# Kernel optimization log

Hardware: AMD Instinct MI355X
Metric: run time of the kernel (lower is better)

The kernel has to match this reference:

```python
import jax, jax.numpy as jnp
import numpy as np

NEG_SLOPE = 0.01
K = 27  # 3x3x3 kernel taps


def conv3d(x, w, b, pad):
    out = jax.lax.conv_general_dilated(
        x, w, window_strides=(1, 1, 1), padding=[(pad, pad)] * 3,
        dimension_numbers=('NCDHW', 'OIDHW', 'NCDHW'))
    return out + b[None, :, None, None, None]


def lrelu(v):
    return jnp.where(v >= 0, v, NEG_SLOPE * v)


def deform_conv3d_hw(x, offsets, w, b):
    # x: [B,C,T,H,W]; offsets: [B,2*K,T,H,W] with (dh, dw) per kernel tap;
    # depth offset is 0 ('HW' mode). Bilinear sampling in H,W, zero pad OOB.
    B, C, T, H, W = x.shape
    off = offsets.reshape(B, K, 2, T, H, W)
    dh, dw = off[:, :, 0], off[:, :, 1]  # [B,K,T,H,W]
    kidx = jnp.arange(K)
    kt = (kidx // 9)[None, :, None, None, None]
    kh = ((kidx // 3) % 3)[None, :, None, None, None]
    kw = (kidx % 3)[None, :, None, None, None]

    t_in = jnp.arange(T)[None, None, :, None, None] - 1 + kt           # int, [1,K,T,1,1]
    h_s = (jnp.arange(H)[None, None, None, :, None] - 1 + kh) + dh     # [B,K,T,H,W]
    w_s = (jnp.arange(W)[None, None, None, None, :] - 1 + kw) + dw

    t_ok = (t_in >= 0) & (t_in < T)
    t_c = jnp.clip(t_in, 0, T - 1)
    t_idx = jnp.broadcast_to(t_c, (B, K, T, H, W))
    t_ok = jnp.broadcast_to(t_ok, (B, K, T, H, W))

    h0 = jnp.floor(h_s); w0 = jnp.floor(w_s)
    fh = h_s - h0; fw = w_s - w0
    h0i = h0.astype(jnp.int32); w0i = w0.astype(jnp.int32)

    def gather_b(xb, ti, hi, wi):
        return xb[:, ti, hi, wi]  # [C,K,T,H,W]
    gather = jax.vmap(gather_b)

    cols = jnp.zeros((B, C, K, T, H, W), x.dtype)
    for ih, wgt_h in ((h0i, 1.0 - fh), (h0i + 1, fh)):
        h_ok = (ih >= 0) & (ih < H)
        ih_c = jnp.clip(ih, 0, H - 1)
        for iw, wgt_w in ((w0i, 1.0 - fw), (w0i + 1, fw)):
            w_ok = (iw >= 0) & (iw < W)
            iw_c = jnp.clip(iw, 0, W - 1)
            mask = (t_ok & h_ok & w_ok).astype(x.dtype)
            wgt = (wgt_h * wgt_w * mask)[:, None]  # [B,1,K,T,H,W]
            cols = cols + wgt * gather(x, t_idx, ih_c, iw_c)
    O = w.shape[0]
    out = jnp.einsum('bckthw,ock->bothw', cols, w.reshape(O, C, K))
    return out + b[None, :, None, None, None]


def setup_inputs() -> dict:
    key = jax.random.key(0)
    ks = jax.random.split(key, 9)
    B, Cin, Cout, T, H, W = 1, 64, 64, 8, 64, 64
    s1 = 1.0 / np.sqrt(Cin * 27)
    sr = 1.0 / np.sqrt(Cin)
    sd = 1.0 / np.sqrt(Cout * 27)
    return {
        'x': jax.random.normal(ks[0], (B, Cin, T, H, W), jnp.float32),
        'W1': jax.random.normal(ks[1], (Cout, Cin, 3, 3, 3), jnp.float32) * s1,
        'b1': jax.random.normal(ks[2], (Cout,), jnp.float32) * s1,
        'W_off': jax.random.normal(ks[3], (2 * K, Cout, 3, 3, 3), jnp.float32) * 0.01,
        'b_off': jax.random.normal(ks[4], (2 * K,), jnp.float32) * 0.01,
        'Wd': jax.random.normal(ks[5], (Cout, Cout, 3, 3, 3), jnp.float32) * sd,
        'bd': jax.random.normal(ks[6], (Cout,), jnp.float32) * sd,
        'Wr': jax.random.normal(ks[7], (Cout, Cin, 1, 1, 1), jnp.float32) * sr,
        'br': jax.random.normal(ks[8], (Cout,), jnp.float32) * sr,
    }


def reference(x, W1, b1, W_off, b_off, Wd, bd, Wr, br):
    y1 = lrelu(conv3d(x, W1, b1, pad=1))
    offsets = conv3d(y1, W_off, b_off, pad=1)          # DeformConvPack offset branch
    y2 = lrelu(deform_conv3d_hw(y1, offsets, Wd, bd))  # deformable conv, 'HW' offsets
    res = conv3d(x, Wr, br, pad=0)                     # 1x1x1 residual conv
    return y2 + res
```

## Files before the change

kernel.cpp:

```cpp
#include <hip/hip_runtime.h>
#include <hip/hip_bf16.h>

#define T_ 8
#define H_ 64
#define W_ 64
#define C_ 64
#define HW_ (H_ * W_)
#define THW_ (T_ * H_ * W_)
#define KTAPS 27
#define KDIM (C_ * KTAPS)
#define NOFF 54
#define OSTR2 58
#define AWC 35
#define AWCP 36

typedef __bf16 bf16x8 __attribute__((ext_vector_type(8)));
typedef float floatx4 __attribute__((ext_vector_type(4)));

#define LGKM_BARRIER()                                        \
    do {                                                      \
        asm volatile("s_waitcnt lgkmcnt(0)" ::: "memory");    \
        __builtin_amdgcn_s_barrier();                         \
    } while (0)

#define DECODE_SWZ_CONV(bid, t, h, wh)                        \
    const int hi3_ = (bid) & 7;                               \
    const int rest_ = (bid) >> 3;                             \
    const int wh = rest_ & 1;                                 \
    const int h = hi3_ * 8 + ((rest_ >> 1) & 7);              \
    const int t = rest_ >> 4;
#define DECODE_SWZ_ROW(bid, t, h)                             \
    const int h = ((bid) & 7) * 8 + (((bid) >> 3) & 7);       \
    const int t = (bid) >> 6;

__global__ __launch_bounds__(256) void prep_tocl_kernel(
    const float* __restrict__ x, __hip_bfloat16* __restrict__ xcl,
    const float* __restrict__ w1, const float* __restrict__ woff,
    const float* __restrict__ wd, const float* __restrict__ wr,
    __hip_bfloat16* __restrict__ w1s, __hip_bfloat16* __restrict__ woffs,
    __hip_bfloat16* __restrict__ wds, __hip_bfloat16* __restrict__ wrs) {
    __shared__ float tile[64][65];
    const int tid = threadIdx.x;

    {
        int i = blockIdx.x * 256 + tid;
        if (i < C_ * KDIM) {
            int j = i & 7, lane = (i >> 3) & 63, s = (i >> 9) & 1, g16 = (i >> 10) & 3, tap = i >> 12;
            int co = g16 * 16 + (lane & 15);
            int cin = s * 32 + (lane >> 4) * 8 + j;
            int src = (co * C_ + cin) * KTAPS + tap;
            w1s[i] = __float2bfloat16(w1[src]);
            woffs[i] = (co < NOFF) ? __float2bfloat16(woff[src]) : __float2bfloat16(0.f);
            wds[i] = __float2bfloat16(wd[src]);
        }
        if (i < C_ * C_) {
            int j = i & 7, lane = (i >> 3) & 63, s = (i >> 9) & 1, g16 = i >> 10;
            int co = g16 * 16 + (lane & 15);
            int cin = s * 32 + (lane >> 4) * 8 + j;
            wrs[i] = __float2bfloat16(wr[co * C_ + cin]);
        }
    }

    const int pos0 = blockIdx.x * 64;
    for (int i = tid; i < 4096; i += 256) {
        int ch = i >> 6, p = i & 63;
        tile[ch][p] = x[ch * THW_ + pos0 + p];
    }
    __syncthreads();
    for (int i = tid; i < 4096; i += 256) {
        int p = i >> 6, ch = i & 63;
        xcl[(pos0 + p) * C_ + ch] = __float2bfloat16(tile[ch][p]);
    }
}

__global__ __launch_bounds__(256) void conv_stream_kernel(
    const __hip_bfloat16* __restrict__ in_cl,
    const __hip_bfloat16* __restrict__ wTs,
    const float* __restrict__ bias,
    __hip_bfloat16* __restrict__ out_cl_b16) {
    __shared__ __hip_bfloat16 ts[32 * 72];
    __shared__ __hip_bfloat16 awin[3 * AWCP * C_];

    const int tid = threadIdx.x;
    const int wv = tid >> 6;
    const int lane = tid & 63;
    const int l15 = lane & 15;
    const int quad = lane >> 4;
    DECODE_SWZ_CONV(blockIdx.x, t, h, wh)
    const int w0 = wh * 32;
    const int pg = wv >> 1;
    const int chf = wv & 1;
    const int wpos = w0 + pg * 16 + l15;
    const int posbase = t * HW_ + h * W_;

    floatx4 acc0 = (floatx4){0.f, 0.f, 0.f, 0.f};
    floatx4 acc1 = (floatx4){0.f, 0.f, 0.f, 0.f};
    const bf16x8 z = {};
    const __hip_bfloat16* wb = wTs + chf * 2048 + lane * 8;

    auto rdwin = [&](int rr, int cc, int chunk) -> bf16x8 {
        const int u = (rr * AWCP + cc) * 8 + (chunk ^ (cc & 7));
        return *(const bf16x8*)((const char*)awin + u * 16);
    };

    const int ktlo = (t == 0) ? 1 : 0;
    const int kthi = (t == T_ - 1) ? 2 : 3;

#pragma unroll 1
    for (int kt = ktlo; kt < kthi; ++kt) {
        const int t_in = t - 1 + kt;

        LGKM_BARRIER();
        for (int i = tid; i < 3 * AWC * 8; i += 256) {
            const int rh = i / (AWC * 8);
            const int rem = i - rh * (AWC * 8);
            const int rw = rem >> 3;
            const int cc = rem & 7;
            const int hsrc = min(max(h - 1 + rh, 0), H_ - 1);
            const int wsrc = min(max(w0 - 1 + rw, 0), W_ - 1);
            const int u = (rh * AWCP + rw) * 8 + (cc ^ (rw & 7));
            *(bf16x8*)((char*)awin + u * 16) =
                *(const bf16x8*)&in_cl[(t_in * HW_ + hsrc * W_ + wsrc) * C_ + cc * 8];
        }
        LGKM_BARRIER();

#pragma unroll 1
        for (int kh = 0; kh < 3; ++kh) {
            const int h_in = h - 1 + kh;
            if ((unsigned)h_in >= H_) continue;
#pragma unroll
            for (int kw = 0; kw < 3; ++kw) {
                const int tap = kt * 9 + kh * 3 + kw;
                const int w_in = wpos - 1 + kw;
                const bool v = (unsigned)w_in < W_;
                const int rw = pg * 16 + l15 + kw;
                bf16x8 a0 = rdwin(kh, rw, quad);
                bf16x8 a1 = rdwin(kh, rw, quad + 4);
                a0 = v ? a0 : z;
                a1 = v ? a1 : z;
                const __hip_bfloat16* bp = wb + tap * 4096;
                const bf16x8 b00 = *(const bf16x8*)(bp);
                const bf16x8 b01 = *(const bf16x8*)(bp + 512);
                const bf16x8 b10 = *(const bf16x8*)(bp + 1024);
                const bf16x8 b11 = *(const bf16x8*)(bp + 1536);
                acc0 = __builtin_amdgcn_mfma_f32_16x16x32_bf16(a0, b00, acc0, 0, 0, 0);
                acc0 = __builtin_amdgcn_mfma_f32_16x16x32_bf16(a1, b01, acc0, 0, 0, 0);
                acc1 = __builtin_amdgcn_mfma_f32_16x16x32_bf16(a0, b10, acc1, 0, 0, 0);
                acc1 = __builtin_amdgcn_mfma_f32_16x16x32_bf16(a1, b11, acc1, 0, 0, 0);
            }
        }
    }

    const int n0 = chf * 32 + l15;
    const float bv0 = bias[n0], bv1 = bias[n0 + 16];
#pragma unroll
    for (int r = 0; r < 4; ++r) {
        const int p = pg * 16 + quad * 4 + r;
        float v0 = acc0[r] + bv0;
        v0 = (v0 >= 0.f) ? v0 : 0.01f * v0;
        float v1 = acc1[r] + bv1;
        v1 = (v1 >= 0.f) ? v1 : 0.01f * v1;
        ts[p * 72 + n0] = __float2bfloat16(v0);
        ts[p * 72 + n0 + 16] = __float2bfloat16(v1);
    }
    __syncthreads();
    {
        const int p = tid >> 3, ck = tid & 7;
        const uint4 v4 = *(const uint4*)&ts[p * 72 + ck * 8];
        *(uint4*)&out_cl_b16[(posbase + w0 + p) * C_ + ck * 8] = v4;
    }
}

struct G2 {
    bf16x8 a[4];
    bf16x8 b[4];
    float w00, w01, w10, w11;
};

__global__ __launch_bounds__(256) void deform_fused_kernel(
    const __hip_bfloat16* __restrict__ y1b,
    const __hip_bfloat16* __restrict__ woffs, const float* __restrict__ boff,
    const __hip_bfloat16* __restrict__ wds, const float* __restrict__ bd,
    const __hip_bfloat16* __restrict__ xclb, const __hip_bfloat16* __restrict__ wrs,
    const float* __restrict__ br, float* __restrict__ out) {
    __shared__ __hip_bfloat16 win[6 * 64 * 64];
    __shared__ float offs[4][16][OSTR2];

    const int tid = threadIdx.x;
    const int wv = tid >> 6;
    const int lane = tid & 63;
    const int l15 = lane & 15;
    const int quad = lane >> 4;
    DECODE_SWZ_ROW(blockIdx.x, t, h)
    const int posbase = t * HW_ + h * W_;
    const int pw = wv * 16 + l15;

    const int ktlo = (t == 0) ? 1 : 0;
    const int kthi = (t == T_ - 1) ? 2 : 3;

    auto rdwin = [&](int rr, int cc, int chunk) -> bf16x8 {
        const int u = (rr * 64 + cc) * 8 + (chunk ^ (cc & 7));
        return *(const bf16x8*)((const char*)win + u * 16);
    };

    {
        floatx4 oacc[4];
#pragma unroll
        for (int g = 0; g < 4; ++g) oacc[g] = (floatx4){0.f, 0.f, 0.f, 0.f};
        const bf16x8 z = {};

#pragma unroll 1
        for (int kt = ktlo; kt < kthi; ++kt) {
            const int tin = t - 1 + kt;

            LGKM_BARRIER();
            for (int i = tid; i < 3 * 64 * 8; i += 256) {
                const int rh = i >> 9;
                const int rem = i & 511;
                const int rw = rem >> 3;
                const int cc = rem & 7;
                const int hsrc = min(max(h - 1 + rh, 0), H_ - 1);
                const int u = (rh * 64 + rw) * 8 + (cc ^ (rw & 7));
                *(bf16x8*)((char*)win + u * 16) =
                    *(const bf16x8*)&y1b[(tin * HW_ + hsrc * W_ + rw) * C_ + cc * 8];
            }
            LGKM_BARRIER();

#pragma unroll 1
            for (int kh = 0; kh < 3; ++kh) {
                const int h_in = h - 1 + kh;
                if ((unsigned)h_in >= H_) continue;
#pragma unroll
                for (int kw = 0; kw < 3; ++kw) {
                    const int tap = kt * 9 + kh * 3 + kw;
                    const int w_in = pw - 1 + kw;
                    const bool v = (unsigned)w_in < W_;
                    const int wc = v ? w_in : 0;
                    bf16x8 a0 = rdwin(kh, wc, quad);
                    bf16x8 a1 = rdwin(kh, wc, quad + 4);
                    a0 = v ? a0 : z;
                    a1 = v ? a1 : z;
                    const __hip_bfloat16* op = woffs + tap * 4096 + lane * 8;
#pragma unroll
                    for (int g = 0; g < 4; ++g) {
                        const bf16x8 b0 = *(const bf16x8*)(op + g * 1024);
                        const bf16x8 b1 = *(const bf16x8*)(op + g * 1024 + 512);
                        oacc[g] = __builtin_amdgcn_mfma_f32_16x16x32_bf16(a0, b0, oacc[g], 0, 0, 0);
                        oacc[g] = __builtin_amdgcn_mfma_f32_16x16x32_bf16(a1, b1, oacc[g], 0, 0, 0);
                    }
                }
            }
        }
#pragma unroll
        for (int g = 0; g < 4; ++g) {
            const int idx = g * 16 + l15;
            if (idx < NOFF) {
                const float bo = boff[idx];
#pragma unroll
                for (int r = 0; r < 4; ++r)
                    offs[wv][quad * 4 + r][idx] = oacc[g][r] + bo;
            }
        }
    }

    floatx4 acc[4], racc[4];
#pragma unroll
    for (int g = 0; g < 4; ++g) {
        acc[g] = (floatx4){0.f, 0.f, 0.f, 0.f};
        racc[g] = (floatx4){0.f, 0.f, 0.f, 0.f};
    }

    {
        const __hip_bfloat16* ap = xclb + (posbase + pw) * C_ + quad * 8;
        const bf16x8 ra0 = *(const bf16x8*)(ap);
        const bf16x8 ra1 = *(const bf16x8*)(ap + 32);
        const __hip_bfloat16* q = wrs + lane * 8;
#pragma unroll
        for (int g = 0; g < 4; ++g) {
            const bf16x8 r0 = *(const bf16x8*)(q + g * 1024);
            const bf16x8 r1 = *(const bf16x8*)(q + g * 1024 + 512);
            racc[g] = __builtin_amdgcn_mfma_f32_16x16x32_bf16(ra0, r0, racc[g], 0, 0, 0);
            racc[g] = __builtin_amdgcn_mfma_f32_16x16x32_bf16(ra1, r1, racc[g], 0, 0, 0);
        }
    }

    auto load_off = [&](int k, float& dh, float& dw) {
        dh = offs[wv][l15][2 * k];
        dw = offs[wv][l15][2 * k + 1];
    };
    auto gatherW = [&](int k, float dh, float dw, G2& g) {
        const int kh = (k / 3) % 3, kw = k % 3;
        const float hs = (float)(h - 1 + kh) + dh;
        const float wsv = (float)(pw - 1 + kw) + dw;
        const float h0f = floorf(hs), w0f = floorf(wsv);
        const float fh = hs - h0f, fw = wsv - w0f;
        const int h0i = (int)h0f, w0i = (int)w0f;
        const int h1i = h0i + 1, w1i = w0i + 1;
        const float m_h0 = ((unsigned)h0i < H_) ? 1.f : 0.f;
        const float m_h1 = ((unsigned)h1i < H_) ? 1.f : 0.f;
        const float m_w0 = ((unsigned)w0i < W_) ? 1.f : 0.f;
        const float m_w1 = ((unsigned)w1i < W_) ? 1.f : 0.f;
        g.w00 = (1.f - fh) * (1.f - fw) * m_h0 * m_w0;
        g.w01 = (1.f - fh) * fw * m_h0 * m_w1;
        g.w10 = fh * (1.f - fw) * m_h1 * m_w0;
        g.w11 = fh * fw * m_h1 * m_w1;
        const int w0c = min(max(w0i, 0), W_ - 1);
        const int w1c = min(max(w1i, 0), W_ - 1);
        const int rh = h0i - (h - 2);
        if ((unsigned)rh <= 4u) {
            g.a[0] = rdwin(rh, w0c, quad);      g.b[0] = rdwin(rh, w0c, quad + 4);
            g.a[1] = rdwin(rh, w1c, quad);      g.b[1] = rdwin(rh, w1c, quad + 4);
            g.a[2] = rdwin(rh + 1, w0c, quad);  g.b[2] = rdwin(rh + 1, w0c, quad + 4);
            g.a[3] = rdwin(rh + 1, w1c, quad);  g.b[3] = rdwin(rh + 1, w1c, quad + 4);
        } else {
            const int h0c = min(max(h0i, 0), H_ - 1);
            const int h1c = min(max(h1i, 0), H_ - 1);
            const int tb = (t - 1 + k / 9) * HW_;
            const __hip_bfloat16* p00 = y1b + (tb + h0c * W_ + w0c) * C_ + quad * 8;
            const __hip_bfloat16* p01 = y1b + (tb + h0c * W_ + w1c) * C_ + quad * 8;
            const __hip_bfloat16* p10 = y1b + (tb + h1c * W_ + w0c) * C_ + quad * 8;
            const __hip_bfloat16* p11 = y1b + (tb + h1c * W_ + w1c) * C_ + quad * 8;
            g.a[0] = *(const bf16x8*)(p00);  g.b[0] = *(const bf16x8*)(p00 + 32);
            g.a[1] = *(const bf16x8*)(p01);  g.b[1] = *(const bf16x8*)(p01 + 32);
            g.a[2] = *(const bf16x8*)(p10);  g.b[2] = *(const bf16x8*)(p10 + 32);
            g.a[3] = *(const bf16x8*)(p11);  g.b[3] = *(const bf16x8*)(p11 + 32);
        }
    };
    auto blend2 = [&](const G2& g, bf16x8& lo, bf16x8& hi) {
        union U { bf16x8 v; __hip_bfloat16 e[8]; };
        U c0, c1, c2, c3, r;
        c0.v = g.a[0]; c1.v = g.a[1]; c2.v = g.a[2]; c3.v = g.a[3];
#pragma unroll
        for (int j = 0; j < 8; ++j) {
            float f = g.w00 * __bfloat162float(c0.e[j]) + g.w01 * __bfloat162float(c1.e[j]) +
                      g.w10 * __bfloat162float(c2.e[j]) + g.w11 * __bfloat162float(c3.e[j]);
            r.e[j] = __float2bfloat16(f);
        }
        lo = r.v;
        c0.v = g.b[0]; c1.v = g.b[1]; c2.v = g.b[2]; c3.v = g.b[3];
#pragma unroll
        for (int j = 0; j < 8; ++j) {
            float f = g.w00 * __bfloat162float(c0.e[j]) + g.w01 * __bfloat162float(c1.e[j]) +
                      g.w10 * __bfloat162float(c2.e[j]) + g.w11 * __bfloat162float(c3.e[j]);
            r.e[j] = __float2bfloat16(f);
        }
        hi = r.v;
    };
    auto tapMFMA = [&](int k, const bf16x8& lo, const bf16x8& hi) {
        const __hip_bfloat16* q = wds + k * 4096 + lane * 8;
#pragma unroll
        for (int g = 0; g < 4; ++g) {
            const bf16x8 b0 = *(const bf16x8*)(q + g * 1024);
            const bf16x8 b1 = *(const bf16x8*)(q + g * 1024 + 512);
            acc[g] = __builtin_amdgcn_mfma_f32_16x16x32_bf16(lo, b0, acc[g], 0, 0, 0);
            acc[g] = __builtin_amdgcn_mfma_f32_16x16x32_bf16(hi, b1, acc[g], 0, 0, 0);
        }
    };

    G2 gA, gB;
#pragma unroll 1
    for (int kt = ktlo; kt < kthi; ++kt) {
        const int tin = t - 1 + kt;
        const int kg = kt * 9;

        LGKM_BARRIER();
        for (int i = tid; i < 6 * 64 * 8; i += 256) {
            const int rh = i >> 9;
            const int rem = i & 511;
            const int rw = rem >> 3;
            const int cc = rem & 7;
            const int hsrc = min(max(h - 2 + rh, 0), H_ - 1);
            const int u = (rh * 64 + rw) * 8 + (cc ^ (rw & 7));
            *(bf16x8*)((char*)win + u * 16) =
                *(const bf16x8*)&y1b[(tin * HW_ + hsrc * W_ + rw) * C_ + cc * 8];
        }
        LGKM_BARRIER();

        {
            float dh, dw;
            load_off(kg, dh, dw);
            gatherW(kg, dh, dw, gA);
        }
        int k = kg;
        for (; k + 1 < kg + 9; k += 2) {
            {
                float dh, dw;
                load_off(k + 1, dh, dw);
                gatherW(k + 1, dh, dw, gB);
                bf16x8 lo, hi;
                blend2(gA, lo, hi);
                tapMFMA(k, lo, hi);
            }
            {
                if (k + 2 < kg + 9) {
                    float dh, dw;
                    load_off(k + 2, dh, dw);
                    gatherW(k + 2, dh, dw, gA);
                }
                bf16x8 lo, hi;
                blend2(gB, lo, hi);
                tapMFMA(k + 1, lo, hi);
            }
        }
        {
            bf16x8 lo, hi;
            blend2(gA, lo, hi);
            tapMFMA(k, lo, hi);
        }
    }

#pragma unroll
    for (int g = 0; g < 4; ++g) {
        const int n = g * 16 + l15;
        const float bdv = bd[n], brv = br[n];
        floatx4 o;
#pragma unroll
        for (int r = 0; r < 4; ++r) {
            float v = acc[g][r] + bdv;
            v = (v >= 0.f) ? v : 0.01f * v;
            o[r] = v + racc[g][r] + brv;
        }
        *(floatx4*)&out[n * THW_ + posbase + wv * 16 + quad * 4] = o;
    }
}

extern "C" void kernel_launch(void* const* d_in, const int* in_sizes, int n_in,
                              void* d_out, int out_size, void* d_ws, size_t ws_size,
                              hipStream_t stream) {
    const float* x    = (const float*)d_in[0];
    const float* W1   = (const float*)d_in[1];
    const float* b1   = (const float*)d_in[2];
    const float* Woff = (const float*)d_in[3];
    const float* boff = (const float*)d_in[4];
    const float* Wd   = (const float*)d_in[5];
    const float* bd   = (const float*)d_in[6];
    const float* Wr   = (const float*)d_in[7];
    const float* br   = (const float*)d_in[8];
    float* out = (float*)d_out;

    float* ws = (float*)d_ws;
    __hip_bfloat16* xclb  = (__hip_bfloat16*)(ws);
    __hip_bfloat16* y1b   = (__hip_bfloat16*)(ws + 1048576);
    __hip_bfloat16* w1s   = (__hip_bfloat16*)(ws + 2097152);
    __hip_bfloat16* woffs = (__hip_bfloat16*)(ws + 2152448);
    __hip_bfloat16* wdsb  = (__hip_bfloat16*)(ws + 2207744);
    __hip_bfloat16* wrsb  = (__hip_bfloat16*)(ws + 2263040);

    prep_tocl_kernel<<<THW_ / 64, 256, 0, stream>>>(
        x, xclb, W1, Woff, Wd, Wr, w1s, woffs, wdsb, wrsb);

    conv_stream_kernel<<<dim3(T_ * H_ * 2), 256, 0, stream>>>(
        xclb, w1s, b1, y1b);

    deform_fused_kernel<<<dim3(T_ * H_), 256, 0, stream>>>(
        y1b, woffs, boff, wdsb, bd, xclb, wrsb, br, out);
}
```

Baseline: 152.1 us.

## Split deformable conv channel reduction across two wave groups with LDS reduce

Doubles the deform kernel block to 512 threads. Each group of four waves handles half of the 64 input channels, for both the offset conv and the deformable/residual MFMAs. Partial accumulators are then reduced through shared memory before the epilogue. The aim is to halve per-thread gather, blend and register work and to raise the number of waves in flight, since only 512 blocks exist. In exchange it adds barriers and an LDS round-trip for the reduction, and the bilinear weight computation is now done redundantly by both groups.

```diff
diff --git a/kernel.cpp b/kernel.cpp
--- a/kernel.cpp
+++ b/kernel.cpp
@@ -171,13 +171,12 @@
     }
 }
 
-struct G2 {
-    bf16x8 a[4];
-    bf16x8 b[4];
+struct G1 {
+    bf16x8 c[4];
     float w00, w01, w10, w11;
 };
 
-__global__ __launch_bounds__(256) void deform_fused_kernel(
+__global__ __launch_bounds__(512, 4) void deform_fused_kernel(
     const __hip_bfloat16* __restrict__ y1b,
     const __hip_bfloat16* __restrict__ woffs, const float* __restrict__ boff,
     const __hip_bfloat16* __restrict__ wds, const float* __restrict__ bd,
@@ -193,10 +192,15 @@
     const int quad = lane >> 4;
     DECODE_SWZ_ROW(blockIdx.x, t, h)
     const int posbase = t * HW_ + h * W_;
-    const int pw = wv * 16 + l15;
+    const int pg = wv & 3;
+    const int kh2 = wv >> 2;
+    const int pw = pg * 16 + l15;
+    const int ch = quad + kh2 * 4;
 
     const int ktlo = (t == 0) ? 1 : 0;
     const int kthi = (t == T_ - 1) ? 2 : 3;
+
+    float* winf = (float*)win;
 
     auto rdwin = [&](int rr, int cc, int chunk) -> bf16x8 {
         const int u = (rr * 64 + cc) * 8 + (chunk ^ (cc & 7));
@@ -214,7 +218,7 @@
             const int tin = t - 1 + kt;
 
             LGKM_BARRIER();
-            for (int i = tid; i < 3 * 64 * 8; i += 256) {
+            for (int i = tid; i < 3 * 64 * 8; i += 512) {
                 const int rh = i >> 9;
                 const int rem = i & 511;
                 const int rw = rem >> 3;
@@ -236,29 +240,36 @@
                     const int w_in = pw - 1 + kw;
                     const bool v = (unsigned)w_in < W_;
                     const int wc = v ? w_in : 0;
-                    bf16x8 a0 = rdwin(kh, wc, quad);
-                    bf16x8 a1 = rdwin(kh, wc, quad + 4);
-                    a0 = v ? a0 : z;
-                    a1 = v ? a1 : z;
-                    const __hip_bfloat16* op = woffs + tap * 4096 + lane * 8;
+                    bf16x8 a = rdwin(kh, wc, ch);
+                    a = v ? a : z;
+                    const __hip_bfloat16* op = woffs + tap * 4096 + kh2 * 512 + lane * 8;
 #pragma unroll
                     for (int g = 0; g < 4; ++g) {
-                        const bf16x8 b0 = *(const bf16x8*)(op + g * 1024);
-                        const bf16x8 b1 = *(const bf16x8*)(op + g * 1024 + 512);
-                        oacc[g] = __builtin_amdgcn_mfma_f32_16x16x32_bf16(a0, b0, oacc[g], 0, 0, 0);
-                        oacc[g] = __builtin_amdgcn_mfma_f32_16x16x32_bf16(a1, b1, oacc[g], 0, 0, 0);
+                        const bf16x8 b = *(const bf16x8*)(op + g * 1024);
+                        oacc[g] = __builtin_amdgcn_mfma_f32_16x16x32_bf16(a, b, oacc[g], 0, 0, 0);
                     }
                 }
             }
         }
-#pragma unroll
-        for (int g = 0; g < 4; ++g) {
-            const int idx = g * 16 + l15;
-            if (idx < NOFF) {
-                const float bo = boff[idx];
-#pragma unroll
-                for (int r = 0; r < 4; ++r)
-                    offs[wv][quad * 4 + r][idx] = oacc[g][r] + bo;
+        LGKM_BARRIER();
+        if (kh2 == 1) {
+#pragma unroll
+            for (int g = 0; g < 4; ++g)
+                *(floatx4*)&winf[(pg * 64 + lane) * 16 + g * 4] = oacc[g];
+        }
+        LGKM_BARRIER();
+        if (kh2 == 0) {
+#pragma unroll
+            for (int g = 0; g < 4; ++g) {
+                const floatx4 p4 = *(const floatx4*)&winf[(pg * 64 + lane) * 16 + g * 4];
+                oacc[g] += p4;
+                const int idx = g * 16 + l15;
+                if (idx < NOFF) {
+                    const float bo = boff[idx];
+#pragma unroll
+                    for (int r = 0; r < 4; ++r)
+                        offs[pg][quad * 4 + r][idx] = oacc[g][r] + bo;
+                }
             }
         }
     }
@@ -271,24 +282,20 @@
     }
 
     {
-        const __hip_bfloat16* ap = xclb + (posbase + pw) * C_ + quad * 8;
-        const bf16x8 ra0 = *(const bf16x8*)(ap);
-        const bf16x8 ra1 = *(const bf16x8*)(ap + 32);
-        const __hip_bfloat16* q = wrs + lane * 8;
+        const bf16x8 ra = *(const bf16x8*)(xclb + (posbase + pw) * C_ + ch * 8);
+        const __hip_bfloat16* q = wrs + kh2 * 512 + lane * 8;
 #pragma unroll
         for (int g = 0; g < 4; ++g) {
             const bf16x8 r0 = *(const bf16x8*)(q + g * 1024);
-            const bf16x8 r1 = *(const bf16x8*)(q + g * 1024 + 512);
-            racc[g] = __builtin_amdgcn_mfma_f32_16x16x32_bf16(ra0, r0, racc[g], 0, 0, 0);
-            racc[g] = __builtin_amdgcn_mfma_f32_16x16x32_bf16(ra1, r1, racc[g], 0, 0, 0);
+            racc[g] = __builtin_amdgcn_mfma_f32_16x16x32_bf16(ra, r0, racc[g], 0, 0, 0);
         }
     }
 
     auto load_off = [&](int k, float& dh, float& dw) {
-        dh = offs[wv][l15][2 * k];
-        dw = offs[wv][l15][2 * k + 1];
-    };
-    auto gatherW = [&](int k, float dh, float dw, G2& g) {
+        dh = offs[pg][l15][2 * k];
+        dw = offs[pg][l15][2 * k + 1];
+    };
+    auto gatherW = [&](int k, float dh, float dw, G1& g) {
         const int kh = (k / 3) % 3, kw = k % 3;
         const float hs = (float)(h - 1 + kh) + dh;
         const float wsv = (float)(pw - 1 + kw) + dw;
@@ -308,63 +315,49 @@
         const int w1c = min(max(w1i, 0), W_ - 1);
         const int rh = h0i - (h - 2);
         if ((unsigned)rh <= 4u) {
-            g.a[0] = rdwin(rh, w0c, quad);      g.b[0] = rdwin(rh, w0c, quad + 4);
-            g.a[1] = rdwin(rh, w1c, quad);      g.b[1] = rdwin(rh, w1c, quad + 4);
-            g.a[2] = rdwin(rh + 1, w0c, quad);  g.b[2] = rdwin(rh + 1, w0c, quad + 4);
-            g.a[3] = rdwin(rh + 1, w1c, quad);  g.b[3] = rdwin(rh + 1, w1c, quad + 4);
+            g.c[0] = rdwin(rh, w0c, ch);
+            g.c[1] = rdwin(rh, w1c, ch);
+            g.c[2] = rdwin(rh + 1, w0c, ch);
+            g.c[3] = rdwin(rh + 1, w1c, ch);
         } else {
             const int h0c = min(max(h0i, 0), H_ - 1);
             const int h1c = min(max(h1i, 0), H_ - 1);
             const int tb = (t - 1 + k / 9) * HW_;
-            const __hip_bfloat16* p00 = y1b + (tb + h0c * W_ + w0c) * C_ + quad * 8;
-            const __hip_bfloat16* p01 = y1b + (tb + h0c * W_ + w1c) * C_ + quad * 8;
-            const __hip_bfloat16* p10 = y1b + (tb + h1c * W_ + w0c) * C_ + quad * 8;
-            const __hip_bfloat16* p11 = y1b + (tb + h1c * W_ + w1c) * C_ + quad * 8;
-            g.a[0] = *(const bf16x8*)(p00);  g.b[0] = *(const bf16x8*)(p00 + 32);
-            g.a[1] = *(const bf16x8*)(p01);  g.b[1] = *(const bf16x8*)(p01 + 32);
-            g.a[2] = *(const bf16x8*)(p10);  g.b[2] = *(const bf16x8*)(p10 + 32);
-            g.a[3] = *(const bf16x8*)(p11);  g.b[3] = *(const bf16x8*)(p11 + 32);
-        }
-    };
-    auto blend2 = [&](const G2& g, bf16x8& lo, bf16x8& hi) {
+            g.c[0] = *(const bf16x8*)(y1b + (tb + h0c * W_ + w0c) * C_ + ch * 8);
+            g.c[1] = *(const bf16x8*)(y1b + (tb + h0c * W_ + w1c) * C_ + ch * 8);
+            g.c[2] = *(const bf16x8*)(y1b + (tb + h1c * W_ + w0c) * C_ + ch * 8);
+            g.c[3] = *(const bf16x8*)(y1b + (tb + h1c * W_ + w1c) * C_ + ch * 8);
+        }
+    };
+    auto blend1 = [&](const G1& g, bf16x8& fr) {
         union U { bf16x8 v; __hip_bfloat16 e[8]; };
         U c0, c1, c2, c3, r;
-        c0.v = g.a[0]; c1.v = g.a[1]; c2.v = g.a[2]; c3.v = g.a[3];
+        c0.v = g.c[0]; c1.v = g.c[1]; c2.v = g.c[2]; c3.v = g.c[3];
 #pragma unroll
         for (int j = 0; j < 8; ++j) {
             float f = g.w00 * __bfloat162float(c0.e[j]) + g.w01 * __bfloat162float(c1.e[j]) +
                       g.w10 * __bfloat162float(c2.e[j]) + g.w11 * __bfloat162float(c3.e[j]);
             r.e[j] = __float2bfloat16(f);
         }
-        lo = r.v;
-        c0.v = g.b[0]; c1.v = g.b[1]; c2.v = g.b[2]; c3.v = g.b[3];
-#pragma unroll
-        for (int j = 0; j < 8; ++j) {
-            float f = g.w00 * __bfloat162float(c0.e[j]) + g.w01 * __bfloat162float(c1.e[j]) +
-                      g.w10 * __bfloat162float(c2.e[j]) + g.w11 * __bfloat162float(c3.e[j]);
-            r.e[j] = __float2bfloat16(f);
-        }
-        hi = r.v;
-    };
-    auto tapMFMA = [&](int k, const bf16x8& lo, const bf16x8& hi) {
-        const __hip_bfloat16* q = wds + k * 4096 + lane * 8;
+        fr = r.v;
+    };
+    auto tapMFMA = [&](int k, const bf16x8& fr) {
+        const __hip_bfloat16* q = wds + k * 4096 + kh2 * 512 + lane * 8;
 #pragma unroll
         for (int g = 0; g < 4; ++g) {
-            const bf16x8 b0 = *(const bf16x8*)(q + g * 1024);
-            const bf16x8 b1 = *(const bf16x8*)(q + g * 1024 + 512);
-            acc[g] = __builtin_amdgcn_mfma_f32_16x16x32_bf16(lo, b0, acc[g], 0, 0, 0);
-            acc[g] = __builtin_amdgcn_mfma_f32_16x16x32_bf16(hi, b1, acc[g], 0, 0, 0);
-        }
-    };
-
-    G2 gA, gB;
+            const bf16x8 b = *(const bf16x8*)(q + g * 1024);
+            acc[g] = __builtin_amdgcn_mfma_f32_16x16x32_bf16(fr, b, acc[g], 0, 0, 0);
+        }
+    };
+
+    G1 gA, gB;
 #pragma unroll 1
     for (int kt = ktlo; kt < kthi; ++kt) {
         const int tin = t - 1 + kt;
         const int kg = kt * 9;
 
         LGKM_BARRIER();
-        for (int i = tid; i < 6 * 64 * 8; i += 256) {
+        for (int i = tid; i < 6 * 64 * 8; i += 512) {
             const int rh = i >> 9;
             const int rem = i & 511;
             const int rw = rem >> 3;
@@ -387,9 +380,9 @@
                 float dh, dw;
                 load_off(k + 1, dh, dw);
                 gatherW(k + 1, dh, dw, gB);
-                bf16x8 lo, hi;
-                blend2(gA, lo, hi);
-                tapMFMA(k, lo, hi);
+                bf16x8 fr;
+                blend1(gA, fr);
+                tapMFMA(k, fr);
             }
             {
                 if (k + 2 < kg + 9) {
@@ -397,30 +390,43 @@
                     load_off(k + 2, dh, dw);
                     gatherW(k + 2, dh, dw, gA);
                 }
-                bf16x8 lo, hi;
-                blend2(gB, lo, hi);
-                tapMFMA(k + 1, lo, hi);
+                bf16x8 fr;
+                blend1(gB, fr);
+                tapMFMA(k + 1, fr);
             }
         }
         {
-            bf16x8 lo, hi;
-            blend2(gA, lo, hi);
-            tapMFMA(k, lo, hi);
-        }
-    }
-
-#pragma unroll
-    for (int g = 0; g < 4; ++g) {
-        const int n = g * 16 + l15;
-        const float bdv = bd[n], brv = br[n];
-        floatx4 o;
-#pragma unroll
-        for (int r = 0; r < 4; ++r) {
-            float v = acc[g][r] + bdv;
-            v = (v >= 0.f) ? v : 0.01f * v;
-            o[r] = v + racc[g][r] + brv;
-        }
-        *(floatx4*)&out[n * THW_ + posbase + wv * 16 + quad * 4] = o;
+            bf16x8 fr;
+            blend1(gA, fr);
+            tapMFMA(k, fr);
+        }
+    }
+
+    LGKM_BARRIER();
+    if (kh2 == 1) {
+#pragma unroll
+        for (int g = 0; g < 4; ++g) {
+            *(floatx4*)&winf[(pg * 64 + lane) * 32 + g * 4] = acc[g];
+            *(floatx4*)&winf[(pg * 64 + lane) * 32 + 16 + g * 4] = racc[g];
+        }
+    }
+    LGKM_BARRIER();
+    if (kh2 == 0) {
+#pragma unroll
+        for (int g = 0; g < 4; ++g) {
+            const floatx4 pa = *(const floatx4*)&winf[(pg * 64 + lane) * 32 + g * 4];
+            const floatx4 pr = *(const floatx4*)&winf[(pg * 64 + lane) * 32 + 16 + g * 4];
+            const int n = g * 16 + l15;
+            const float bdv = bd[n], brv = br[n];
+            floatx4 o;
+#pragma unroll
+            for (int r = 0; r < 4; ++r) {
+                float v = acc[g][r] + pa[r] + bdv;
+                v = (v >= 0.f) ? v : 0.01f * v;
+                o[r] = v + racc[g][r] + pr[r] + brv;
+            }
+            *(floatx4*)&out[n * THW_ + posbase + pg * 16 + quad * 4] = o;
+        }
     }
 }
 
@@ -452,6 +458,6 @@
     conv_stream_kernel<<<dim3(T_ * H_ * 2), 256, 0, stream>>>(
         xclb, w1s, b1, y1b);
 
-    deform_fused_kernel<<<dim3(T_ * H_), 256, 0, stream>>>(
+    deform_fused_kernel<<<dim3(T_ * H_), 512, 0, stream>>>(
         y1b, woffs, boff, wdsb, bd, xclb, wrsb, br, out);
 }
```

Result: no change. 150.7 us (-0.9%).
